# Kernel optimization log

Hardware: AMD Instinct MI355X
Metric: run time of the kernel (lower is better)

## Reference

```python
import jax, jax.numpy as jnp
import numpy as np

H, DN, DR, DV, L = 16, 128, 64, 128, 512
EPS = 1e-6

def rotate_half(x):
    x1, x2 = jnp.split(x, 2, axis=-1)
    return jnp.concatenate((-x2, x1), axis=-1)

def setup_inputs() -> dict:
    key = jax.random.key(0)
    ks = jax.random.split(key, 8)
    B, S, HID = 2, 2048, 2048
    inv_freq = 1.0 / (10000.0 ** (jnp.arange(0, DR, 2, dtype=jnp.float32) / DR))
    pos = jnp.arange(B * S, dtype=jnp.float32)
    freqs = pos[:, None] * inv_freq[None, :]
    emb = jnp.concatenate((freqs, freqs), axis=-1)
    return {
        "hidden_states": jax.random.normal(ks[0], (B, S, HID), jnp.float32),
        "cos": jnp.cos(emb),
        "sin": jnp.sin(emb),
        "q_proj_w": jax.random.normal(ks[1], (H * (DN + DR), HID), jnp.float32) * 0.02,
        "kv_a_proj_w": jax.random.normal(ks[2], (L + DR, HID), jnp.float32) * 0.02,
        "kv_a_ln_w": jnp.ones((L,), jnp.float32),
        "W_UK_T": jax.random.normal(ks[3], (H, DN, L), jnp.float32) * 0.02,
        "W_UV": jax.random.normal(ks[4], (H, L, DV), jnp.float32) * 0.02,
        "o_proj_w": jax.random.normal(ks[5], (HID, H * DV), jnp.float32) * 0.02,
    }

def reference(hidden_states, cos, sin, q_proj_w, kv_a_proj_w, kv_a_ln_w, W_UK_T, W_UV, o_proj_w):
    B, S, HID = hidden_states.shape
    T = B * S
    x = hidden_states.reshape(T, HID)
    # q projection -> [T, H, DN+DR]
    q = (x @ q_proj_w.T).reshape(T, H, DN + DR)
    q_pass, q_rot = q[..., :DN], q[..., DN:]
    # compressed kv -> latent + rope key (MQA-style, shared across heads)
    ckv = x @ kv_a_proj_w.T  # [T, L+DR]
    k_pass, k_rot = ckv[..., :L], ckv[..., L:]
    kv_c = k_pass * jax.lax.rsqrt(jnp.mean(k_pass * k_pass, axis=-1, keepdims=True) + EPS) * kv_a_ln_w
    # interleaved RoPE (rope_interleave=True): de-interleave then rotate_half form
    q_rot = q_rot.reshape(T, H, DR // 2, 2).swapaxes(-1, -2).reshape(T, H, DR)
    k_rot = k_rot.reshape(T, DR // 2, 2).swapaxes(-1, -2).reshape(T, DR)
    q_rot = q_rot * cos[:, None, :] + rotate_half(q_rot) * sin[:, None, :]
    k_rot = k_rot * cos + rotate_half(k_rot) * sin
    # absorb W_UK into queries: [T,H,L]
    q_lat = jnp.einsum('thd,hdl->thl', q_pass, W_UK_T)
    q_lat = q_lat.reshape(B, S, H, L)
    q_rot = q_rot.reshape(B, S, H, DR)
    kv_c_b = kv_c.reshape(B, S, L)
    k_rot_b = k_rot.reshape(B, S, DR)
    scale = 1.0 / np.sqrt(DN + DR)
    scores = (jnp.einsum('bshl,btl->bhst', q_lat, kv_c_b)
              + jnp.einsum('bshd,btd->bhst', q_rot, k_rot_b)) * scale
    causal = jnp.tril(jnp.ones((S, S), dtype=bool))
    scores = jnp.where(causal[None, None], scores, jnp.float32(-1e30))
    attn = jax.nn.softmax(scores, axis=-1)
    out_lat = jnp.einsum('bhst,btl->bshl', attn, kv_c_b)   # [B,S,H,L]
    out = jnp.einsum('bshl,hlv->bshv', out_lat, W_UV)       # [B,S,H,DV]
    out = out.reshape(B, S, H * DV) @ o_proj_w.T
    return out
```

## Files before the change

kernel.cpp:

```cpp
#include <hip/hip_runtime.h>
#include <stdint.h>

#define T_TOK 4096
#define HIDD  2048
#define NH    16
#define DNN   128
#define DRR   64
#define DVV   128
#define LAT   512
#define DQK   576
#define SEQ   2048
#define NB    2
#define KSTR  592
#define KCH   2368
#define QCKV  3712

typedef __attribute__((__ext_vector_type__(8))) short short8;
typedef __attribute__((__ext_vector_type__(4))) float f32x4;

__device__ __forceinline__ float bf2f(ushort u) {
  union { uint32_t i; float f; } v; v.i = ((uint32_t)u) << 16; return v.f;
}
__device__ __forceinline__ ushort f2bf(float f) {
  union { float f; uint32_t i; } v; v.f = f;
  uint32_t r = v.i + 0x7FFF + ((v.i >> 16) & 1);
  return (ushort)(r >> 16);
}

__device__ __forceinline__ void gld_lds16(const void* g, void* l) {
  __builtin_amdgcn_global_load_lds((const __attribute__((address_space(1))) void*)g,
                                   (__attribute__((address_space(3))) void*)l, 16, 0, 0);
}

__global__ void cast_all(const float* __restrict__ hs, const float* __restrict__ qw,
                         const float* __restrict__ kvw, const float* __restrict__ wuk,
                         const float* __restrict__ wuv, const float* __restrict__ wo,
                         ushort* __restrict__ xb, ushort* __restrict__ wq_b,
                         ushort* __restrict__ wkv_b, ushort* __restrict__ outk,
                         ushort* __restrict__ outv, ushort* __restrict__ outo) {
  const int bx = blockIdx.x;
  if (bx < 8192) {
    int i = bx * 256 + threadIdx.x;
    float4 v = ((const float4*)hs)[i];
    ushort4 o; o.x = f2bf(v.x); o.y = f2bf(v.y); o.z = f2bf(v.z); o.w = f2bf(v.w);
    ((ushort4*)xb)[i] = o;
  } else if (bx < 14336) {
    int i = (bx - 8192) * 256 + threadIdx.x;
    float4 v = ((const float4*)qw)[i];
    ushort4 o; o.x = f2bf(v.x); o.y = f2bf(v.y); o.z = f2bf(v.z); o.w = f2bf(v.w);
    ((ushort4*)wq_b)[i] = o;
  } else if (bx < 15616) {
    int i = (bx - 14336) * 256 + threadIdx.x;
    int row = (i * 4) >> 11;
    ushort4 o;
    if (row < 576) {
      float4 v = ((const float4*)kvw)[i];
      o.x = f2bf(v.x); o.y = f2bf(v.y); o.z = f2bf(v.z); o.w = f2bf(v.w);
    } else { o.x = 0; o.y = 0; o.z = 0; o.w = 0; }
    ((ushort4*)wkv_b)[i] = o;
  } else if (bx < 19712) {
    int o = (bx - 15616) * 256 + threadIdx.x;
    int d = o & 127, l = (o >> 7) & 511, h = o >> 16;
    outk[o] = f2bf(wuk[((size_t)(h * 128 + d)) * 512 + l]);
  } else if (bx < 23808) {
    int o = (bx - 19712) * 256 + threadIdx.x;
    int l = o & 511, v = (o >> 9) & 127, h = o >> 16;
    outv[o] = f2bf(wuv[((size_t)(h * 512 + l)) * 128 + v]);
  } else {
    int i = (bx - 23808) * 256 + threadIdx.x;
    float4 v = ((const float4*)wo)[i];
    ushort4 o; o.x = f2bf(v.x); o.y = f2bf(v.y); o.z = f2bf(v.z); o.w = f2bf(v.w);
    ((ushort4*)outo)[i] = o;
  }
}

template<int OUT_BF16>
__global__ __launch_bounds__(256) void gemm_bt(
    const ushort* __restrict__ A, const ushort* __restrict__ B, void* __restrict__ Cv,
    int K, int lda, int ldb, int ldc,
    long long aB, long long bB, long long cB)
{
  __shared__ ushort As[2][128 * 32];
  __shared__ ushort Bs[2][128 * 32];
  const int tid = threadIdx.x;
  const int lane = tid & 63, wid = tid >> 6;

  const int gx = gridDim.x;
  const int nwg = gx * gridDim.y;
  int l = blockIdx.y * gx + blockIdx.x;
  int tile = l;
  if ((nwg & 7) == 0) tile = (l & 7) * (nwg >> 3) + (l >> 3);
  const int m0 = (tile / gx) * 128, n0 = (tile % gx) * 128;

  A += (size_t)blockIdx.z * aB;
  B += (size_t)blockIdx.z * bB;
  const int wm = (wid >> 1) * 64, wn = (wid & 1) * 64;
  const int fr = lane & 15;
  const int kk = (lane >> 4) * 8;

  auto stage = [&](int k0, int buf) {
#pragma unroll
    for (int i = 0; i < 2; ++i) {
      int c = i * 256 + tid;
      gld_lds16(A + (size_t)(m0 + (c >> 2)) * lda + k0 + (c & 3) * 8, (void*)(&As[buf][0] + c * 8));
    }
#pragma unroll
    for (int i = 0; i < 2; ++i) {
      int c = i * 256 + tid;
      gld_lds16(B + (size_t)(n0 + (c >> 2)) * ldb + k0 + (c & 3) * 8, (void*)(&Bs[buf][0] + c * 8));
    }
  };

  f32x4 acc[4][4] = {};
  const int nt = K >> 5;
  stage(0, 0);
  for (int t = 0; t < nt; ++t) {
    const int cur = t & 1;
    if (t + 1 < nt) {
      stage((t + 1) << 5, cur ^ 1);
      asm volatile("s_waitcnt vmcnt(4)" ::: "memory");
    } else {
      asm volatile("s_waitcnt vmcnt(0)" ::: "memory");
    }
    __builtin_amdgcn_sched_barrier(0);
    __builtin_amdgcn_s_barrier();
    __builtin_amdgcn_sched_barrier(0);

    short8 af[4], bf[4];
#pragma unroll
    for (int x = 0; x < 4; ++x) af[x] = *(const short8*)(&As[cur][0] + (wm + x * 16 + fr) * 32 + kk);
#pragma unroll
    for (int x = 0; x < 4; ++x) bf[x] = *(const short8*)(&Bs[cur][0] + (wn + x * 16 + fr) * 32 + kk);
#pragma unroll
    for (int mi = 0; mi < 4; ++mi)
#pragma unroll
      for (int ni = 0; ni < 4; ++ni)
        acc[mi][ni] = __builtin_amdgcn_mfma_f32_16x16x32_bf16(af[mi], bf[ni], acc[mi][ni], 0, 0, 0);

    __builtin_amdgcn_sched_barrier(0);
    __builtin_amdgcn_s_barrier();
    __builtin_amdgcn_sched_barrier(0);
  }

  const int rb = (lane >> 4) * 4;
#pragma unroll
  for (int mi = 0; mi < 4; ++mi)
#pragma unroll
    for (int ni = 0; ni < 4; ++ni)
#pragma unroll
      for (int r = 0; r < 4; ++r) {
        size_t row = (size_t)(m0 + wm + mi * 16 + rb + r);
        size_t col = (size_t)(n0 + wn + ni * 16 + fr);
        size_t idx = row * (size_t)ldc + col + (size_t)blockIdx.z * cB;
        if (OUT_BF16) ((ushort*)Cv)[idx] = f2bf(acc[mi][ni][r]);
        else          ((float*)Cv)[idx]  = acc[mi][ni][r];
      }
}

__global__ __launch_bounds__(256) void gemm_k128(
    const ushort* __restrict__ A, const ushort* __restrict__ B, ushort* __restrict__ C,
    int lda, int ldb, int ldc,
    long long aB, long long bB, long long cB)
{
  __shared__ ushort As[4][128 * 32];
  __shared__ ushort Bs[4][128 * 32];
  const int tid = threadIdx.x;
  const int lane = tid & 63, wid = tid >> 6;

  const int gx = gridDim.x;
  const int nwg = gx * gridDim.y;
  int l = blockIdx.y * gx + blockIdx.x;
  int tile = l;
  if ((nwg & 7) == 0) tile = (l & 7) * (nwg >> 3) + (l >> 3);
  const int m0 = (tile / gx) * 128, n0 = (tile % gx) * 128;

  A += (size_t)blockIdx.z * aB;
  B += (size_t)blockIdx.z * bB;
  const int wm = (wid >> 1) * 64, wn = (wid & 1) * 64;
  const int fr = lane & 15;
  const int kk = (lane >> 4) * 8;

#pragma unroll
  for (int kc = 0; kc < 4; ++kc) {
#pragma unroll
    for (int i = 0; i < 2; ++i) {
      int c = i * 256 + tid;
      gld_lds16(A + (size_t)(m0 + (c >> 2)) * lda + kc * 32 + (c & 3) * 8, (void*)(&As[kc][0] + c * 8));
    }
#pragma unroll
    for (int i = 0; i < 2; ++i) {
      int c = i * 256 + tid;
      gld_lds16(B + (size_t)(n0 + (c >> 2)) * ldb + kc * 32 + (c & 3) * 8, (void*)(&Bs[kc][0] + c * 8));
    }
  }
  asm volatile("s_waitcnt vmcnt(0)" ::: "memory");
  __builtin_amdgcn_sched_barrier(0);
  __builtin_amdgcn_s_barrier();
  __builtin_amdgcn_sched_barrier(0);

  f32x4 acc[4][4] = {};
#pragma unroll
  for (int kc = 0; kc < 4; ++kc) {
    short8 af[4], bf[4];
#pragma unroll
    for (int x = 0; x < 4; ++x) af[x] = *(const short8*)(&As[kc][0] + (wm + x * 16 + fr) * 32 + kk);
#pragma unroll
    for (int x = 0; x < 4; ++x) bf[x] = *(const short8*)(&Bs[kc][0] + (wn + x * 16 + fr) * 32 + kk);
#pragma unroll
    for (int mi = 0; mi < 4; ++mi)
#pragma unroll
      for (int ni = 0; ni < 4; ++ni)
        acc[mi][ni] = __builtin_amdgcn_mfma_f32_16x16x32_bf16(af[mi], bf[ni], acc[mi][ni], 0, 0, 0);
  }

  const int rb = (lane >> 4) * 4;
#pragma unroll
  for (int mi = 0; mi < 4; ++mi)
#pragma unroll
    for (int ni = 0; ni < 4; ++ni)
#pragma unroll
      for (int r = 0; r < 4; ++r) {
        size_t row = (size_t)(m0 + wm + mi * 16 + rb + r);
        size_t col = (size_t)(n0 + wn + ni * 16 + fr);
        C[row * (size_t)ldc + col + (size_t)blockIdx.z * cB] = f2bf(acc[mi][ni][r]);
      }
}

__global__ __launch_bounds__(256) void rms_rope_kq(
    const ushort* __restrict__ qckv, const float* __restrict__ lnw,
    const float* __restrict__ cosb, const float* __restrict__ sinb,
    ushort* __restrict__ k_eff, ushort* __restrict__ q_eff)
{
  const int t = blockIdx.x, tid = threadIdx.x;
  __shared__ float red[4];
  const size_t base = (size_t)t * QCKV + 3072;
  float v0 = bf2f(qckv[base + tid]);
  float v1 = bf2f(qckv[base + 256 + tid]);
  float ss = v0 * v0 + v1 * v1;
#pragma unroll
  for (int m = 1; m < 64; m <<= 1) ss += __shfl_xor(ss, m);
  if ((tid & 63) == 0) red[tid >> 6] = ss;

#pragma unroll
  for (int i = 0; i < 4; ++i) {
    int item = i * 256 + tid;
    int hh = item >> 6, j = item & 63;
    size_t qb = (size_t)t * QCKV + hh * 192 + 128;
    int src  = (j < 32) ? 2 * j : 2 * (j - 32) + 1;
    int psrc = (j < 32) ? src + 1 : src - 1;
    float xv = bf2f(qckv[qb + src]), pv = bf2f(qckv[qb + psrc]);
    float c = cosb[t * 64 + j], s = sinb[t * 64 + j];
    q_eff[((size_t)hh * T_TOK + t) * DQK + 512 + j] = f2bf((j < 32) ? xv * c - pv * s : xv * c + pv * s);
  }

  __syncthreads();
  float rn = rsqrtf((red[0] + red[1] + red[2] + red[3]) * (1.0f / 512.0f) + 1e-6f);
  k_eff[(size_t)t * KSTR + tid]       = f2bf(v0 * rn * lnw[tid]);
  k_eff[(size_t)t * KSTR + 256 + tid] = f2bf(v1 * rn * lnw[256 + tid]);
  if (tid < 64) {
    int j = tid;
    int src  = (j < 32) ? 2 * j : 2 * (j - 32) + 1;
    int psrc = (j < 32) ? src + 1 : src - 1;
    float xv = bf2f(qckv[base + 512 + src]);
    float pv = bf2f(qckv[base + 512 + psrc]);
    float c = cosb[t * 64 + j], s = sinb[t * 64 + j];
    k_eff[(size_t)t * KSTR + 512 + j] = f2bf((j < 32) ? xv * c - pv * s : xv * c + pv * s);
  }
}

__global__ __launch_bounds__(256) void transpose_kv(
    const ushort* __restrict__ keff, ushort* __restrict__ kvT)
{
  __shared__ ushort Tl[64][72];
  const int s0 = blockIdx.x * 64, v0 = blockIdx.y * 64, b = blockIdx.z;
  const int tid = threadIdx.x;
#pragma unroll
  for (int i = 0; i < 2; ++i) {
    int c = i * 256 + tid;
    int r = c >> 3, c8 = (c & 7) * 8;
    *(short8*)&Tl[r][c8] = *(const short8*)&keff[((size_t)b * SEQ + s0 + r) * KSTR + v0 + c8];
  }
  __syncthreads();
#pragma unroll
  for (int i = 0; i < 2; ++i) {
    int c = i * 256 + tid;
    int v = c >> 3, s8 = (c & 7) * 8;
    short8 o;
#pragma unroll
    for (int e = 0; e < 8; ++e) o[e] = Tl[s8 + e][v];
    *(short8*)&kvT[((size_t)b * 512 + v0 + v) * SEQ + s0 + s8] = o;
  }
}

__global__ __launch_bounds__(512, 2) void attn3(
    const ushort* __restrict__ q_eff, const ushort* __restrict__ keff,
    const ushort* __restrict__ kvT, ushort* __restrict__ out_lat)
{
  const int pair = blockIdx.x;
  const int h = blockIdx.y, b = blockIdx.z;
  const int tid = threadIdx.x, lane = tid & 63, w = tid >> 6;
  __shared__ ushort Ks[2][32 * KSTR];
  __shared__ ushort Vt[2][512 * 32];
  __shared__ ushort Pl[8][16 * 40];

  const int fr = lane & 15, g = lane >> 4;

  auto stageK = [&](int kt, int buf) {
    const ushort* ksrc = keff + ((size_t)b * SEQ + (size_t)kt * 32) * KSTR;
    ushort* kd = &Ks[buf][0];
#pragma unroll
    for (int i = 0; i < 5; ++i) {
      int c0 = w * 320 + i * 64;
      if (c0 < KCH) {
        int c = c0 + lane;
        gld_lds16(ksrc + (size_t)c * 8, (void*)(kd + (size_t)c * 8));
      }
    }
  };
  auto stageV = [&](int kt, int buf) {
    const ushort* vsrc = kvT + (size_t)b * 512 * SEQ + (size_t)kt * 32;
    ushort* vd = &Vt[buf][0];
#pragma unroll
    for (int i = 0; i < 4; ++i) {
      int c = w * 256 + i * 64 + lane;
      gld_lds16(vsrc + (size_t)(c >> 2) * SEQ + (c & 3) * 8, (void*)(vd + (size_t)c * 8));
    }
  };

  for (int half = 0; half < 2; ++half) {
    const int qb = half ? pair : (15 - pair);
    const int q0 = qb * 128 + w * 16;

    const ushort* qrow = q_eff + ((size_t)h * T_TOK + (size_t)b * SEQ + q0 + fr) * DQK + g * 8;
    short8 qf[18];
#pragma unroll
    for (int ks = 0; ks < 18; ++ks) qf[ks] = *(const short8*)(qrow + ks * 32);

    f32x4 acc[32] = {};
    float m_s[4] = {-1e30f, -1e30f, -1e30f, -1e30f};
    float l_s[4] = {0.f, 0.f, 0.f, 0.f};

    const int nt = 4 * qb + 4;

    stageK(0, 0);
    stageV(0, 0);

    for (int kt = 0; kt < nt; ++kt) {
      const int cur = kt & 1;
      if (kt + 1 < nt) {
        stageK(kt + 1, cur ^ 1);
        stageV(kt + 1, cur ^ 1);
        if (w == 7) asm volatile("s_waitcnt vmcnt(6)" ::: "memory");
        else        asm volatile("s_waitcnt vmcnt(9)" ::: "memory");
      } else {
        asm volatile("s_waitcnt vmcnt(0)" ::: "memory");
      }
      __builtin_amdgcn_sched_barrier(0);
      __builtin_amdgcn_s_barrier();
      __builtin_amdgcn_sched_barrier(0);

      if (kt * 32 <= q0 + 15) {
        const ushort* Kc = &Ks[cur][0];
        const ushort* Vc = &Vt[cur][0];
        f32x4 s0 = {}, s1 = {};
        __builtin_amdgcn_s_setprio(1);
#pragma unroll
        for (int ks = 0; ks < 18; ++ks) {
          short8 b0 = *(const short8*)(Kc + (0 * 16 + fr) * KSTR + ks * 32 + g * 8);
          short8 b1 = *(const short8*)(Kc + (1 * 16 + fr) * KSTR + ks * 32 + g * 8);
          s0 = __builtin_amdgcn_mfma_f32_16x16x32_bf16(qf[ks], b0, s0, 0, 0, 0);
          s1 = __builtin_amdgcn_mfma_f32_16x16x32_bf16(qf[ks], b1, s1, 0, 0, 0);
        }
        __builtin_amdgcn_s_setprio(0);
        const float SC = 0.07216878364870322f;
        const bool diag = (kt * 32 + 31 > q0);
        float sv0[4], sv1[4];
#pragma unroll
        for (int r = 0; r < 4; ++r) {
          int qg = q0 + 4 * g + r;
          float a0 = s0[r] * SC, a1 = s1[r] * SC;
          if (diag) {
            if (kt * 32 + fr > qg)      a0 = -1e30f;
            if (kt * 32 + 16 + fr > qg) a1 = -1e30f;
          }
          sv0[r] = a0; sv1[r] = a1;
        }
        float mx[4];
#pragma unroll
        for (int r = 0; r < 4; ++r) {
          float m2 = fmaxf(sv0[r], sv1[r]);
          m2 = fmaxf(m2, __shfl_xor(m2, 1));
          m2 = fmaxf(m2, __shfl_xor(m2, 2));
          m2 = fmaxf(m2, __shfl_xor(m2, 4));
          m2 = fmaxf(m2, __shfl_xor(m2, 8));
          mx[r] = m2;
        }
        float need = mx[0] - m_s[0];
#pragma unroll
        for (int r = 1; r < 4; ++r) need = fmaxf(need, mx[r] - m_s[r]);
        if (__any(need > 8.0f)) {
          float rsc[4];
#pragma unroll
          for (int r = 0; r < 4; ++r) {
            float mn = fmaxf(m_s[r], mx[r]);
            rsc[r] = __expf(m_s[r] - mn);
            m_s[r] = mn;
            l_s[r] *= rsc[r];
          }
#pragma unroll
          for (int n2 = 0; n2 < 32; ++n2)
#pragma unroll
            for (int r = 0; r < 4; ++r) acc[n2][r] *= rsc[r];
        }
        float p0[4], p1[4];
#pragma unroll
        for (int r = 0; r < 4; ++r) {
          p0[r] = __expf(sv0[r] - m_s[r]);
          p1[r] = __expf(sv1[r] - m_s[r]);
          float ps = p0[r] + p1[r];
          ps += __shfl_xor(ps, 1);
          ps += __shfl_xor(ps, 2);
          ps += __shfl_xor(ps, 4);
          ps += __shfl_xor(ps, 8);
          l_s[r] += ps;
          Pl[w][(4 * g + r) * 40 + fr]      = f2bf(p0[r]);
          Pl[w][(4 * g + r) * 40 + 16 + fr] = f2bf(p1[r]);
        }
        short8 pa = *(const short8*)(Pl[w] + fr * 40 + g * 8);
        __builtin_amdgcn_s_setprio(1);
#pragma unroll
        for (int n2 = 0; n2 < 32; ++n2) {
          short8 bv = *(const short8*)(Vc + (n2 * 16 + fr) * 32 + g * 8);
          acc[n2] = __builtin_amdgcn_mfma_f32_16x16x32_bf16(pa, bv, acc[n2], 0, 0, 0);
        }
        __builtin_amdgcn_s_setprio(0);
      }
      __builtin_amdgcn_sched_barrier(0);
      __builtin_amdgcn_s_barrier();
      __builtin_amdgcn_sched_barrier(0);
    }

    const size_t obase = ((size_t)h * T_TOK + (size_t)b * SEQ + q0) * LAT;
    float inv[4];
#pragma unroll
    for (int r = 0; r < 4; ++r) inv[r] = 1.0f / l_s[r];
#pragma unroll
    for (int n2 = 0; n2 < 32; ++n2)
#pragma unroll
      for (int r = 0; r < 4; ++r)
        out_lat[obase + (size_t)(4 * g + r) * LAT + n2 * 16 + fr] = f2bf(acc[n2][r] * inv[r]);
  }
}

extern "C" void kernel_launch(void* const* d_in, const int* in_sizes, int n_in,
                              void* d_out, int out_size, void* d_ws, size_t ws_size,
                              hipStream_t stream) {
  const float* hs   = (const float*)d_in[0];
  const float* cosb = (const float*)d_in[1];
  const float* sinb = (const float*)d_in[2];
  const float* qw   = (const float*)d_in[3];
  const float* kvw  = (const float*)d_in[4];
  const float* lnw  = (const float*)d_in[5];
  const float* wuk  = (const float*)d_in[6];
  const float* wuv  = (const float*)d_in[7];
  const float* wo   = (const float*)d_in[8];
  float* out = (float*)d_out;
  char* ws = (char*)d_ws;

  const size_t o_xb   = 0;
  const size_t o_qb   = 16777216;
  const size_t o_wq   = 47185920;
  const size_t o_wkv  = 59768832;
  const size_t o_ol   = 0;
  const size_t o_wukt = 67108864;
  const size_t o_wuvt = 69206016;
  const size_t o_wo   = 71303168;
  const size_t o_keff = 79691776;
  const size_t o_qeff = 84541440;
  const size_t o_oh   = 160038912;
  const size_t o_kvt  = 176816128;

  ushort* xb    = (ushort*)(ws + o_xb);
  ushort* qbuf  = (ushort*)(ws + o_qb);
  ushort* wq_b  = (ushort*)(ws + o_wq);
  ushort* wkv_b = (ushort*)(ws + o_wkv);
  ushort* olat  = (ushort*)(ws + o_ol);
  ushort* wukt  = (ushort*)(ws + o_wukt);
  ushort* wuvt  = (ushort*)(ws + o_wuvt);
  ushort* wo_b  = (ushort*)(ws + o_wo);
  ushort* keff  = (ushort*)(ws + o_keff);
  ushort* qeff  = (ushort*)(ws + o_qeff);
  ushort* ohead = (ushort*)(ws + o_oh);
  ushort* kvt   = (ushort*)(ws + o_kvt);

  cast_all<<<27904, 256, 0, stream>>>(hs, qw, kvw, wuk, wuv, wo,
                                      xb, wq_b, wkv_b, wukt, wuvt, wo_b);

  gemm_bt<1><<<dim3(29, 32, 1), 256, 0, stream>>>(xb, wq_b, qbuf, 2048, 2048, 2048, QCKV, 0, 0, 0);
  rms_rope_kq<<<4096, 256, 0, stream>>>(qbuf, lnw, cosb, sinb, keff, qeff);
  transpose_kv<<<dim3(32, 8, 2), 256, 0, stream>>>(keff, kvt);
  gemm_k128<<<dim3(4, 32, 16), 256, 0, stream>>>(qbuf, wukt, qeff, QCKV, 128, 576,
                                                 192LL, 65536LL, 2359296LL);
  attn3<<<dim3(8, 16, 2), 512, 0, stream>>>(qeff, keff, kvt, olat);
  gemm_bt<1><<<dim3(1, 32, 16), 256, 0, stream>>>(olat, wuvt, ohead, 512, 512, 512, 2048,
                                                  2097152LL, 65536LL, 128LL);
  gemm_bt<0><<<dim3(16, 32, 1), 256, 0, stream>>>(ohead, wo_b, out, 2048, 2048, 2048, 2048, 0, 0, 0);
}
```

Baseline: 607.0 us.

## Fuse W_UV up-projection into attention epilogue, dropping out_lat round trip

The attention kernel's epilogue now normalises the latent accumulators, stages them through per-wave LDS as bf16 A-fragments, and multiplies by the per-head W_UV slice with MFMA. The result is written directly into the per-head output buffer. This removes the separate batched W_UV GEMM launch and the write and re-read of the 4096x16x512 latent output. In exchange, each wave reads W_UV straight from global memory without LDS sharing, which adds epilogue latency and register pressure to the attention kernel.

```diff
diff --git a/kernel.cpp b/kernel.cpp
--- a/kernel.cpp
+++ b/kernel.cpp
@@ -294,7 +294,8 @@
 
 __global__ __launch_bounds__(512, 2) void attn3(
     const ushort* __restrict__ q_eff, const ushort* __restrict__ keff,
-    const ushort* __restrict__ kvT, ushort* __restrict__ out_lat)
+    const ushort* __restrict__ kvT, const ushort* __restrict__ wuvt,
+    ushort* __restrict__ ohead)
 {
   const int pair = blockIdx.x;
   const int h = blockIdx.y, b = blockIdx.z;
@@ -440,15 +441,37 @@
       __builtin_amdgcn_sched_barrier(0);
     }
 
-    const size_t obase = ((size_t)h * T_TOK + (size_t)b * SEQ + q0) * LAT;
-    float inv[4];
-#pragma unroll
-    for (int r = 0; r < 4; ++r) inv[r] = 1.0f / l_s[r];
-#pragma unroll
-    for (int n2 = 0; n2 < 32; ++n2)
-#pragma unroll
-      for (int r = 0; r < 4; ++r)
-        out_lat[obase + (size_t)(4 * g + r) * LAT + n2 * 16 + fr] = f2bf(acc[n2][r] * inv[r]);
+    {
+      const ushort* wv = wuvt + (size_t)h * 65536;
+      float inv[4];
+#pragma unroll
+      for (int r = 0; r < 4; ++r) inv[r] = 1.0f / l_s[r];
+      f32x4 acc2[8] = {};
+#pragma unroll
+      for (int kc = 0; kc < 16; ++kc) {
+#pragma unroll
+        for (int r = 0; r < 4; ++r) {
+          Pl[w][(4 * g + r) * 40 + fr]      = f2bf(acc[2 * kc][r]     * inv[r]);
+          Pl[w][(4 * g + r) * 40 + 16 + fr] = f2bf(acc[2 * kc + 1][r] * inv[r]);
+        }
+        asm volatile("s_waitcnt lgkmcnt(0)" ::: "memory");
+        __builtin_amdgcn_sched_barrier(0);
+        short8 af = *(const short8*)(Pl[w] + fr * 40 + g * 8);
+#pragma unroll
+        for (int n = 0; n < 8; ++n) {
+          short8 bv = *(const short8*)(wv + (size_t)(n * 16 + fr) * 512 + kc * 32 + g * 8);
+          acc2[n] = __builtin_amdgcn_mfma_f32_16x16x32_bf16(af, bv, acc2[n], 0, 0, 0);
+        }
+        asm volatile("s_waitcnt lgkmcnt(0)" ::: "memory");
+        __builtin_amdgcn_sched_barrier(0);
+      }
+      const size_t orow0 = (size_t)b * SEQ + q0;
+#pragma unroll
+      for (int n = 0; n < 8; ++n)
+#pragma unroll
+        for (int r = 0; r < 4; ++r)
+          ohead[(orow0 + 4 * g + r) * 2048 + h * 128 + n * 16 + fr] = f2bf(acc2[n][r]);
+    }
   }
 }
 
@@ -471,7 +494,6 @@
   const size_t o_qb   = 16777216;
   const size_t o_wq   = 47185920;
   const size_t o_wkv  = 59768832;
-  const size_t o_ol   = 0;
   const size_t o_wukt = 67108864;
   const size_t o_wuvt = 69206016;
   const size_t o_wo   = 71303168;
@@ -484,7 +506,6 @@
   ushort* qbuf  = (ushort*)(ws + o_qb);
   ushort* wq_b  = (ushort*)(ws + o_wq);
   ushort* wkv_b = (ushort*)(ws + o_wkv);
-  ushort* olat  = (ushort*)(ws + o_ol);
   ushort* wukt  = (ushort*)(ws + o_wukt);
   ushort* wuvt  = (ushort*)(ws + o_wuvt);
   ushort* wo_b  = (ushort*)(ws + o_wo);
@@ -501,8 +522,6 @@
   transpose_kv<<<dim3(32, 8, 2), 256, 0, stream>>>(keff, kvt);
   gemm_k128<<<dim3(4, 32, 16), 256, 0, stream>>>(qbuf, wukt, qeff, QCKV, 128, 576,
                                                  192LL, 65536LL, 2359296LL);
-  attn3<<<dim3(8, 16, 2), 512, 0, stream>>>(qeff, keff, kvt, olat);
-  gemm_bt<1><<<dim3(1, 32, 16), 256, 0, stream>>>(olat, wuvt, ohead, 512, 512, 512, 2048,
-                                                  2097152LL, 65536LL, 128LL);
+  attn3<<<dim3(8, 16, 2), 512, 0, stream>>>(qeff, keff, kvt, wuvt, ohead);
   gemm_bt<0><<<dim3(16, 32, 1), 256, 0, stream>>>(ohead, wo_b, out, 2048, 2048, 2048, 2048, 0, 0, 0);
 }
```

New measurement: 758.7 us. 25.0% more time.
